# Kernel optimization log

Measured on AMD Instinct MI355X. Metric: run time of the kernel, lower is better.

## Reference

```python
import jax, jax.numpy as jnp
import numpy as np

B, NQ, NK, D, H = 2, 1024, 1024, 512, 32


def setup_inputs() -> dict:
    key = jax.random.key(0)
    ks = jax.random.split(key, 6)
    keys_t = jax.random.normal(ks[0], (B, NK, D), dtype=jnp.float32)
    queries = jax.random.normal(ks[1], (B, NQ, D), dtype=jnp.float32)
    # torch nn.Linear default init: U(-1/sqrt(fan_in), 1/sqrt(fan_in))
    s1 = 1.0 / np.sqrt(2 * D)
    W1 = jax.random.uniform(ks[2], (2 * D, H), jnp.float32, -s1, s1)  # (2d, hidden)
    b1 = jax.random.uniform(ks[3], (H,), jnp.float32, -s1, s1)
    s2 = 1.0 / np.sqrt(H)
    W2 = jax.random.uniform(ks[4], (H, 1), jnp.float32, -s2, s2)
    b2 = jax.random.uniform(ks[5], (1,), jnp.float32, -s2, s2)
    return {"keys": keys_t, "queries": queries, "W1": W1, "b1": b1, "W2": W2, "b2": b2}


def reference(keys, queries, W1, b1, W2, b2):
    # logits[b,q,k] = W2 . tanh(W1 @ cat(keys[b,k], queries[b,q]) + b1) + b2
    # Decompose first linear: cat(k,q) @ W1 == k @ W1[:D] + q @ W1[D:]
    d = keys.shape[-1]
    hk = jnp.einsum('bkd,dh->bkh', keys, W1[:d])      # (B, NK, H)
    hq = jnp.einsum('bqd,dh->bqh', queries, W1[d:])   # (B, NQ, H)
    h = jnp.tanh(hk[:, None, :, :] + hq[:, :, None, :] + b1)  # (B, NQ, NK, H)
    logits = jnp.einsum('bqkh,ho->bqko', h, W2)[..., 0] + b2[0]  # (B, NQ, NK)
    return logits
```

## Files before the change

### kernel.cpp

```cpp
#include <hip/hip_runtime.h>
#include <hip/hip_bf16.h>

#define NB 2
#define NQS 1024
#define NKS 1024
#define DD 512
#define HH 32
#define NKROW (NB * NKS)
#define W1S 34

typedef __attribute__((ext_vector_type(8))) short bf16x8;
typedef __attribute__((ext_vector_type(4))) float f32x4;

static __device__ __forceinline__ float fexp2(float x) {
#if __has_builtin(__builtin_amdgcn_exp2f)
  return __builtin_amdgcn_exp2f(x);
#else
  float r; asm("v_exp_f32 %0, %1" : "=v"(r) : "v"(x)); return r;
#endif
}
static __device__ __forceinline__ float frcp(float x) {
#if __has_builtin(__builtin_amdgcn_rcpf)
  return __builtin_amdgcn_rcpf(x);
#else
  float r; asm("v_rcp_f32 %0, %1" : "=v"(r) : "v"(x)); return r;
#endif
}
static __device__ __forceinline__ float rfl_f32(float x) {
  return __int_as_float(__builtin_amdgcn_readfirstlane(__float_as_int(x)));
}

__global__ __launch_bounds__(256) void p1_proj_mfma(
    const float* __restrict__ keys, const float* __restrict__ queries,
    const float* __restrict__ W1, const float* __restrict__ b1,
    float* __restrict__ E) {
  __shared__ __hip_bfloat16 W1L[DD * W1S];
  __shared__ float red[4 * 2 * 64 * 4];
  const float S = 2.8853900817779268f;
  const int tid = threadIdx.x;
  const int row0 = blockIdx.x * 16;
  const bool isq = row0 >= NKROW;
  const float* src = isq ? queries + (size_t)(row0 - NKROW) * DD
                         : keys + (size_t)row0 * DD;
  const float* w1 = W1 + (isq ? (size_t)DD * HH : 0);
#pragma unroll
  for (int s = 0; s < 16; ++s) {
    const int f = tid + s * 256;
    float4 v = *(const float4*)(w1 + (size_t)f * 4);
    const int k = f >> 3, h0 = (f & 7) * 4;
    __hip_bfloat16* p = &W1L[k * W1S + h0];
    p[0] = __float2bfloat16(v.x); p[1] = __float2bfloat16(v.y);
    p[2] = __float2bfloat16(v.z); p[3] = __float2bfloat16(v.w);
  }
  __syncthreads();
  const int l = tid & 63, w = tid >> 6;
  const int m = l & 15, kq = l >> 4;
  f32x4 acc0 = {0.f, 0.f, 0.f, 0.f}, acc1 = {0.f, 0.f, 0.f, 0.f};
  const float* arow = src + (size_t)m * DD + w * 128 + kq * 8;
  union Frag { bf16x8 v; __hip_bfloat16 e[8]; };
#pragma unroll
  for (int s = 0; s < 4; ++s) {
    const int kb = w * 128 + s * 32;
    float4 a0 = *(const float4*)(arow + s * 32);
    float4 a1 = *(const float4*)(arow + s * 32 + 4);
    Frag af, bf0, bf1;
    af.e[0] = __float2bfloat16(a0.x); af.e[1] = __float2bfloat16(a0.y);
    af.e[2] = __float2bfloat16(a0.z); af.e[3] = __float2bfloat16(a0.w);
    af.e[4] = __float2bfloat16(a1.x); af.e[5] = __float2bfloat16(a1.y);
    af.e[6] = __float2bfloat16(a1.z); af.e[7] = __float2bfloat16(a1.w);
    const __hip_bfloat16* bp = &W1L[(kb + kq * 8) * W1S + m];
#pragma unroll
    for (int j = 0; j < 8; ++j) {
      bf0.e[j] = bp[j * W1S];
      bf1.e[j] = bp[j * W1S + 16];
    }
    acc0 = __builtin_amdgcn_mfma_f32_16x16x32_bf16(af.v, bf0.v, acc0, 0, 0, 0);
    acc1 = __builtin_amdgcn_mfma_f32_16x16x32_bf16(af.v, bf1.v, acc1, 0, 0, 0);
  }
  *(f32x4*)(&red[((w * 2 + 0) * 64 + l) * 4]) = acc0;
  *(f32x4*)(&red[((w * 2 + 1) * 64 + l) * 4]) = acc1;
  __syncthreads();
#pragma unroll
  for (int u = 0; u < 2; ++u) {
    const int o = tid + u * 256;
    const int rr = o >> 5, h = o & 31;
    const int tt = h >> 4, mm = h & 15;
    const int ll = ((rr >> 2) << 4) | mm, r = rr & 3;
    float sum = red[(0 + tt) * 256 + ll * 4 + r] + red[(2 + tt) * 256 + ll * 4 + r] +
                red[(4 + tt) * 256 + ll * 4 + r] + red[(6 + tt) * 256 + ll * 4 + r];
    if (isq) sum += b1[h];
    E[(size_t)(row0 + rr) * HH + h] = fexp2(S * sum);
  }
}

__global__ __launch_bounds__(256, 4) void p2_score(
    const float* __restrict__ E, const float* __restrict__ W2,
    const float* __restrict__ b2, float* __restrict__ out) {
  const int tid = threadIdx.x;
  const int kl = tid & 63;
  const int qg = __builtin_amdgcn_readfirstlane(tid >> 6);
  const int k0 = blockIdx.x * 64, q0 = blockIdx.y * 32, b = blockIdx.z;
  float w2v[HH];
  float c0 = rfl_f32(b2[0]);
#pragma unroll
  for (int h = 0; h < HH; ++h) {
    w2v[h] = rfl_f32(W2[h]);
    c0 += w2v[h];
  }
  const float* ekp = E + (size_t)(b * NKS + k0 + kl) * HH;
  float acc[8];
#pragma unroll
  for (int j = 0; j < 8; ++j) acc[j] = c0;
#pragma unroll
  for (int half = 0; half < 2; ++half) {
    float ek[16];
#pragma unroll
    for (int i = 0; i < 4; ++i) {
      float4 v = *(const float4*)(ekp + half * 16 + i * 4);
      ek[i * 4 + 0] = v.x; ek[i * 4 + 1] = v.y;
      ek[i * 4 + 2] = v.z; ek[i * 4 + 3] = v.w;
    }
    const float* eqb =
        E + ((size_t)NKROW + (size_t)b * NQS + q0 + qg * 8) * HH + half * 16;
#pragma unroll
    for (int j = 0; j < 8; ++j) {
      const float* ej = eqb + (size_t)j * HH;
      float a0 = 0.f, a1 = 0.f;
#pragma unroll
      for (int i2 = 0; i2 < 4; ++i2) {
        float4 ev = *(const float4*)(ej + i2 * 4);
        const int hb = half * 16 + i2 * 4;
        {
          float da = fmaf(ek[i2 * 4 + 0], ev.x, 1.f);
          float db = fmaf(ek[i2 * 4 + 1], ev.y, 1.f);
          float num = fmaf(w2v[hb + 0], db, w2v[hb + 1] * da);
          a0 = fmaf(num, frcp(da * db), a0);
        }
        {
          float da = fmaf(ek[i2 * 4 + 2], ev.z, 1.f);
          float db = fmaf(ek[i2 * 4 + 3], ev.w, 1.f);
          float num = fmaf(w2v[hb + 2], db, w2v[hb + 3] * da);
          a1 = fmaf(num, frcp(da * db), a1);
        }
      }
      acc[j] = fmaf(-2.f, a0 + a1, acc[j]);
    }
  }
  float* outp = out + ((size_t)b * NQS + q0 + qg * 8) * NKS + k0 + kl;
#pragma unroll
  for (int j = 0; j < 8; ++j) outp[(size_t)j * NKS] = acc[j];
}

extern "C" void kernel_launch(void* const* d_in, const int* in_sizes, int n_in,
                              void* d_out, int out_size, void* d_ws, size_t ws_size,
                              hipStream_t stream) {
  const float* keys = (const float*)d_in[0];
  const float* queries = (const float*)d_in[1];
  const float* W1 = (const float*)d_in[2];
  const float* b1 = (const float*)d_in[3];
  const float* W2 = (const float*)d_in[4];
  const float* b2 = (const float*)d_in[5];
  float* out = (float*)d_out;
  float* ws = (float*)d_ws;

  hipLaunchKernelGGL(p1_proj_mfma, dim3(256), dim3(256), 0, stream,
                     keys, queries, W1, b1, ws);
  hipLaunchKernelGGL(p2_score, dim3(NKS / 64, NQS / 32, NB), dim3(256), 0, stream,
                     ws, W2, b2, out);
}
```

Before: 22.09 us.

## Fuse projection and scoring into one kernel with per-tile recomputed projections

Merges the projection kernel and the score kernel into a single launch. Each block projects its own 64 keys and 64 queries into shared memory with MFMA, then computes a 64x64 output tile, with a swizzled block order. This removes one launch and the global workspace round trip, but every block recomputes projections that other blocks share and re-stages W1 twice, which greatly increases redundant loads and MFMA work.

```diff
diff --git a/kernel.cpp b/kernel.cpp
--- a/kernel.cpp
+++ b/kernel.cpp
@@ -6,8 +6,8 @@
 #define NKS 1024
 #define DD 512
 #define HH 32
-#define NKROW (NB * NKS)
 #define W1S 34
+#define EKS 36
 
 typedef __attribute__((ext_vector_type(8))) short bf16x8;
 typedef __attribute__((ext_vector_type(4))) float f32x4;
@@ -30,76 +30,77 @@
   return __int_as_float(__builtin_amdgcn_readfirstlane(__float_as_int(x)));
 }
 
-__global__ __launch_bounds__(256) void p1_proj_mfma(
+__global__ __launch_bounds__(256) void fused_all(
     const float* __restrict__ keys, const float* __restrict__ queries,
     const float* __restrict__ W1, const float* __restrict__ b1,
-    float* __restrict__ E) {
+    const float* __restrict__ W2, const float* __restrict__ b2,
+    float* __restrict__ out) {
   __shared__ __hip_bfloat16 W1L[DD * W1S];
-  __shared__ float red[4 * 2 * 64 * 4];
+  __shared__ float EkL[64 * EKS];
+  __shared__ float EqL[64 * HH];
   const float S = 2.8853900817779268f;
   const int tid = threadIdx.x;
-  const int row0 = blockIdx.x * 16;
-  const bool isq = row0 >= NKROW;
-  const float* src = isq ? queries + (size_t)(row0 - NKROW) * DD
-                         : keys + (size_t)row0 * DD;
-  const float* w1 = W1 + (isq ? (size_t)DD * HH : 0);
-#pragma unroll
-  for (int s = 0; s < 16; ++s) {
-    const int f = tid + s * 256;
-    float4 v = *(const float4*)(w1 + (size_t)f * 4);
-    const int k = f >> 3, h0 = (f & 7) * 4;
-    __hip_bfloat16* p = &W1L[k * W1S + h0];
-    p[0] = __float2bfloat16(v.x); p[1] = __float2bfloat16(v.y);
-    p[2] = __float2bfloat16(v.z); p[3] = __float2bfloat16(v.w);
-  }
-  __syncthreads();
+  const int bid = blockIdx.x;
+  const int swz = (bid & 7) * 64 + (bid >> 3);
+  const int kt = swz >> 5, rem = swz & 31;
+  const int qt = rem >> 1, b = rem & 1;
   const int l = tid & 63, w = tid >> 6;
   const int m = l & 15, kq = l >> 4;
-  f32x4 acc0 = {0.f, 0.f, 0.f, 0.f}, acc1 = {0.f, 0.f, 0.f, 0.f};
-  const float* arow = src + (size_t)m * DD + w * 128 + kq * 8;
   union Frag { bf16x8 v; __hip_bfloat16 e[8]; };
+
 #pragma unroll
-  for (int s = 0; s < 4; ++s) {
-    const int kb = w * 128 + s * 32;
-    float4 a0 = *(const float4*)(arow + s * 32);
-    float4 a1 = *(const float4*)(arow + s * 32 + 4);
-    Frag af, bf0, bf1;
-    af.e[0] = __float2bfloat16(a0.x); af.e[1] = __float2bfloat16(a0.y);
-    af.e[2] = __float2bfloat16(a0.z); af.e[3] = __float2bfloat16(a0.w);
-    af.e[4] = __float2bfloat16(a1.x); af.e[5] = __float2bfloat16(a1.y);
-    af.e[6] = __float2bfloat16(a1.z); af.e[7] = __float2bfloat16(a1.w);
-    const __hip_bfloat16* bp = &W1L[(kb + kq * 8) * W1S + m];
+  for (int phase = 0; phase < 2; ++phase) {
+    const float* w1 = W1 + (size_t)phase * DD * HH;
 #pragma unroll
-    for (int j = 0; j < 8; ++j) {
-      bf0.e[j] = bp[j * W1S];
-      bf1.e[j] = bp[j * W1S + 16];
+    for (int s = 0; s < 16; ++s) {
+      const int f = tid + s * 256;
+      float4 v = *(const float4*)(w1 + (size_t)f * 4);
+      const int k = f >> 3, h0 = (f & 7) * 4;
+      __hip_bfloat16* p = &W1L[k * W1S + h0];
+      p[0] = __float2bfloat16(v.x); p[1] = __float2bfloat16(v.y);
+      p[2] = __float2bfloat16(v.z); p[3] = __float2bfloat16(v.w);
     }
-    acc0 = __builtin_amdgcn_mfma_f32_16x16x32_bf16(af.v, bf0.v, acc0, 0, 0, 0);
-    acc1 = __builtin_amdgcn_mfma_f32_16x16x32_bf16(af.v, bf1.v, acc1, 0, 0, 0);
+    __syncthreads();
+    const float* src = phase ? queries + (size_t)(b * NQS + qt * 64 + w * 16 + m) * DD
+                             : keys + (size_t)(b * NKS + kt * 64 + w * 16 + m) * DD;
+    const float* arow = src + kq * 8;
+    f32x4 acc0 = {0.f, 0.f, 0.f, 0.f}, acc1 = {0.f, 0.f, 0.f, 0.f};
+#pragma unroll
+    for (int s = 0; s < 16; ++s) {
+      float4 a0 = *(const float4*)(arow + s * 32);
+      float4 a1 = *(const float4*)(arow + s * 32 + 4);
+      Frag af, bf0, bf1;
+      af.e[0] = __float2bfloat16(a0.x); af.e[1] = __float2bfloat16(a0.y);
+      af.e[2] = __float2bfloat16(a0.z); af.e[3] = __float2bfloat16(a0.w);
+      af.e[4] = __float2bfloat16(a1.x); af.e[5] = __float2bfloat16(a1.y);
+      af.e[6] = __float2bfloat16(a1.z); af.e[7] = __float2bfloat16(a1.w);
+      const __hip_bfloat16* bp = &W1L[(s * 32 + kq * 8) * W1S + m];
+#pragma unroll
+      for (int j = 0; j < 8; ++j) {
+        bf0.e[j] = bp[j * W1S];
+        bf1.e[j] = bp[j * W1S + 16];
+      }
+      acc0 = __builtin_amdgcn_mfma_f32_16x16x32_bf16(af.v, bf0.v, acc0, 0, 0, 0);
+      acc1 = __builtin_amdgcn_mfma_f32_16x16x32_bf16(af.v, bf1.v, acc1, 0, 0, 0);
+    }
+    if (phase == 0) {
+#pragma unroll
+      for (int r = 0; r < 4; ++r) {
+        const int rr = w * 16 + kq * 4 + r;
+        EkL[rr * EKS + m] = fexp2(S * acc0[r]);
+        EkL[rr * EKS + 16 + m] = fexp2(S * acc1[r]);
+      }
+    } else {
+      const float bias0 = b1[m], bias1 = b1[16 + m];
+#pragma unroll
+      for (int r = 0; r < 4; ++r) {
+        const int rr = w * 16 + kq * 4 + r;
+        EqL[rr * HH + m] = fexp2(S * (acc0[r] + bias0));
+        EqL[rr * HH + 16 + m] = fexp2(S * (acc1[r] + bias1));
+      }
+    }
+    __syncthreads();
   }
-  *(f32x4*)(&red[((w * 2 + 0) * 64 + l) * 4]) = acc0;
-  *(f32x4*)(&red[((w * 2 + 1) * 64 + l) * 4]) = acc1;
-  __syncthreads();
-#pragma unroll
-  for (int u = 0; u < 2; ++u) {
-    const int o = tid + u * 256;
-    const int rr = o >> 5, h = o & 31;
-    const int tt = h >> 4, mm = h & 15;
-    const int ll = ((rr >> 2) << 4) | mm, r = rr & 3;
-    float sum = red[(0 + tt) * 256 + ll * 4 + r] + red[(2 + tt) * 256 + ll * 4 + r] +
-                red[(4 + tt) * 256 + ll * 4 + r] + red[(6 + tt) * 256 + ll * 4 + r];
-    if (isq) sum += b1[h];
-    E[(size_t)(row0 + rr) * HH + h] = fexp2(S * sum);
-  }
-}
-
-__global__ __launch_bounds__(256, 4) void p2_score(
-    const float* __restrict__ E, const float* __restrict__ W2,
-    const float* __restrict__ b2, float* __restrict__ out) {
-  const int tid = threadIdx.x;
-  const int kl = tid & 63;
-  const int qg = __builtin_amdgcn_readfirstlane(tid >> 6);
-  const int k0 = blockIdx.x * 64, q0 = blockIdx.y * 32, b = blockIdx.z;
   float w2v[HH];
   float c0 = rfl_f32(b2[0]);
 #pragma unroll
@@ -107,48 +108,39 @@
     w2v[h] = rfl_f32(W2[h]);
     c0 += w2v[h];
   }
-  const float* ekp = E + (size_t)(b * NKS + k0 + kl) * HH;
-  float acc[8];
+  const int kl = l;
+  float ek[HH];
 #pragma unroll
-  for (int j = 0; j < 8; ++j) acc[j] = c0;
+  for (int i = 0; i < 8; ++i) {
+    float4 v = *(const float4*)(&EkL[kl * EKS + i * 4]);
+    ek[i * 4 + 0] = v.x; ek[i * 4 + 1] = v.y;
+    ek[i * 4 + 2] = v.z; ek[i * 4 + 3] = v.w;
+  }
+  float* outp = out + ((size_t)b * NQS + qt * 64 + w * 16) * NKS + kt * 64 + kl;
+#pragma unroll 4
+  for (int j = 0; j < 16; ++j) {
+    const float* ej = &EqL[(w * 16 + j) * HH];
+    float a0 = 0.f, a1 = 0.f;
 #pragma unroll
-  for (int half = 0; half < 2; ++half) {
-    float ek[16];
-#pragma unroll
-    for (int i = 0; i < 4; ++i) {
-      float4 v = *(const float4*)(ekp + half * 16 + i * 4);
-      ek[i * 4 + 0] = v.x; ek[i * 4 + 1] = v.y;
-      ek[i * 4 + 2] = v.z; ek[i * 4 + 3] = v.w;
+    for (int i2 = 0; i2 < 8; ++i2) {
+      float4 ev = *(const float4*)(ej + i2 * 4);
+      {
+        const int hb = i2 * 4;
+        float da = fmaf(ek[hb + 0], ev.x, 1.f);
+        float db = fmaf(ek[hb + 1], ev.y, 1.f);
+        float num = fmaf(w2v[hb + 0], db, w2v[hb + 1] * da);
+        a0 = fmaf(num, frcp(da * db), a0);
+      }
+      {
+        const int hb = i2 * 4 + 2;
+        float da = fmaf(ek[hb + 0], ev.z, 1.f);
+        float db = fmaf(ek[hb + 1], ev.w, 1.f);
+        float num = fmaf(w2v[hb + 0], db, w2v[hb + 1] * da);
+        a1 = fmaf(num, frcp(da * db), a1);
+      }
     }
-    const float* eqb =
-        E + ((size_t)NKROW + (size_t)b * NQS + q0 + qg * 8) * HH + half * 16;
-#pragma unroll
-    for (int j = 0; j < 8; ++j) {
-      const float* ej = eqb + (size_t)j * HH;
-      float a0 = 0.f, a1 = 0.f;
-#pragma unroll
-      for (int i2 = 0; i2 < 4; ++i2) {
-        float4 ev = *(const float4*)(ej + i2 * 4);
-        const int hb = half * 16 + i2 * 4;
-        {
-          float da = fmaf(ek[i2 * 4 + 0], ev.x, 1.f);
-          float db = fmaf(ek[i2 * 4 + 1], ev.y, 1.f);
-          float num = fmaf(w2v[hb + 0], db, w2v[hb + 1] * da);
-          a0 = fmaf(num, frcp(da * db), a0);
-        }
-        {
-          float da = fmaf(ek[i2 * 4 + 2], ev.z, 1.f);
-          float db = fmaf(ek[i2 * 4 + 3], ev.w, 1.f);
-          float num = fmaf(w2v[hb + 2], db, w2v[hb + 3] * da);
-          a1 = fmaf(num, frcp(da * db), a1);
-        }
-      }
-      acc[j] = fmaf(-2.f, a0 + a1, acc[j]);
-    }
+    outp[(size_t)j * NKS] = fmaf(-2.f, a0 + a1, c0);
   }
-  float* outp = out + ((size_t)b * NQS + q0 + qg * 8) * NKS + k0 + kl;
-#pragma unroll
-  for (int j = 0; j < 8; ++j) outp[(size_t)j * NKS] = acc[j];
 }
 
 extern "C" void kernel_launch(void* const* d_in, const int* in_sizes, int n_in,
@@ -161,10 +153,7 @@
   const float* W2 = (const float*)d_in[4];
   const float* b2 = (const float*)d_in[5];
   float* out = (float*)d_out;
-  float* ws = (float*)d_ws;
 
-  hipLaunchKernelGGL(p1_proj_mfma, dim3(256), dim3(256), 0, stream,
-                     keys, queries, W1, b1, ws);
-  hipLaunchKernelGGL(p2_score, dim3(NKS / 64, NQS / 32, NB), dim3(256), 0, stream,
-                     ws, W2, b2, out);
+  hipLaunchKernelGGL(fused_all, dim3(512), dim3(256), 0, stream,
+                     keys, queries, W1, b1, W2, b2, out);
 }
```

New measurement: 30.79 us. 39.4% more time.

## Split projection K-dimension across blocks and halve per-block query tile in scoring

Applied to the files above, without the earlier changes.

The projection kernel is split into a partial stage where each block handles one 128-wide chunk of the reduction dimension (1024 blocks instead of 256), plus a separate finish kernel that sums the four partials, adds bias and applies exp2. The scoring kernel now processes 16 queries per block instead of 32, doubling the grid, and applies the constant and -2 scale at store time. The aim is more parallelism and better CU fill on the small projection, and higher occupancy in scoring. In exchange it adds a kernel launch and an extra global round trip for the partial sums, and each scoring block reloads key data for less work.

```diff
diff --git a/kernel.cpp b/kernel.cpp
--- a/kernel.cpp
+++ b/kernel.cpp
@@ -30,21 +30,20 @@
   return __int_as_float(__builtin_amdgcn_readfirstlane(__float_as_int(x)));
 }
 
-__global__ __launch_bounds__(256) void p1_proj_mfma(
+__global__ __launch_bounds__(256) void p1a_partial(
     const float* __restrict__ keys, const float* __restrict__ queries,
-    const float* __restrict__ W1, const float* __restrict__ b1,
-    float* __restrict__ E) {
-  __shared__ __hip_bfloat16 W1L[DD * W1S];
+    const float* __restrict__ W1, float* __restrict__ Epart) {
+  __shared__ __hip_bfloat16 W1L[128 * W1S];
   __shared__ float red[4 * 2 * 64 * 4];
-  const float S = 2.8853900817779268f;
   const int tid = threadIdx.x;
-  const int row0 = blockIdx.x * 16;
+  const int rt = blockIdx.x >> 2, kc = blockIdx.x & 3;
+  const int row0 = rt * 16;
   const bool isq = row0 >= NKROW;
   const float* src = isq ? queries + (size_t)(row0 - NKROW) * DD
                          : keys + (size_t)row0 * DD;
-  const float* w1 = W1 + (isq ? (size_t)DD * HH : 0);
+  const float* w1 = W1 + (isq ? (size_t)DD * HH : 0) + (size_t)kc * 128 * HH;
 #pragma unroll
-  for (int s = 0; s < 16; ++s) {
+  for (int s = 0; s < 4; ++s) {
     const int f = tid + s * 256;
     float4 v = *(const float4*)(w1 + (size_t)f * 4);
     const int k = f >> 3, h0 = (f & 7) * 4;
@@ -55,28 +54,24 @@
   __syncthreads();
   const int l = tid & 63, w = tid >> 6;
   const int m = l & 15, kq = l >> 4;
-  f32x4 acc0 = {0.f, 0.f, 0.f, 0.f}, acc1 = {0.f, 0.f, 0.f, 0.f};
-  const float* arow = src + (size_t)m * DD + w * 128 + kq * 8;
   union Frag { bf16x8 v; __hip_bfloat16 e[8]; };
+  const float* arow = src + (size_t)m * DD + kc * 128 + w * 32 + kq * 8;
+  float4 a0 = *(const float4*)(arow);
+  float4 a1 = *(const float4*)(arow + 4);
+  Frag af, bf0, bf1;
+  af.e[0] = __float2bfloat16(a0.x); af.e[1] = __float2bfloat16(a0.y);
+  af.e[2] = __float2bfloat16(a0.z); af.e[3] = __float2bfloat16(a0.w);
+  af.e[4] = __float2bfloat16(a1.x); af.e[5] = __float2bfloat16(a1.y);
+  af.e[6] = __float2bfloat16(a1.z); af.e[7] = __float2bfloat16(a1.w);
+  const __hip_bfloat16* bp = &W1L[(w * 32 + kq * 8) * W1S + m];
 #pragma unroll
-  for (int s = 0; s < 4; ++s) {
-    const int kb = w * 128 + s * 32;
-    float4 a0 = *(const float4*)(arow + s * 32);
-    float4 a1 = *(const float4*)(arow + s * 32 + 4);
-    Frag af, bf0, bf1;
-    af.e[0] = __float2bfloat16(a0.x); af.e[1] = __float2bfloat16(a0.y);
-    af.e[2] = __float2bfloat16(a0.z); af.e[3] = __float2bfloat16(a0.w);
-    af.e[4] = __float2bfloat16(a1.x); af.e[5] = __float2bfloat16(a1.y);
-    af.e[6] = __float2bfloat16(a1.z); af.e[7] = __float2bfloat16(a1.w);
-    const __hip_bfloat16* bp = &W1L[(kb + kq * 8) * W1S + m];
-#pragma unroll
-    for (int j = 0; j < 8; ++j) {
-      bf0.e[j] = bp[j * W1S];
-      bf1.e[j] = bp[j * W1S + 16];
-    }
-    acc0 = __builtin_amdgcn_mfma_f32_16x16x32_bf16(af.v, bf0.v, acc0, 0, 0, 0);
-    acc1 = __builtin_amdgcn_mfma_f32_16x16x32_bf16(af.v, bf1.v, acc1, 0, 0, 0);
+  for (int j = 0; j < 8; ++j) {
+    bf0.e[j] = bp[j * W1S];
+    bf1.e[j] = bp[j * W1S + 16];
   }
+  f32x4 z = {0.f, 0.f, 0.f, 0.f};
+  f32x4 acc0 = __builtin_amdgcn_mfma_f32_16x16x32_bf16(af.v, bf0.v, z, 0, 0, 0);
+  f32x4 acc1 = __builtin_amdgcn_mfma_f32_16x16x32_bf16(af.v, bf1.v, z, 0, 0, 0);
   *(f32x4*)(&red[((w * 2 + 0) * 64 + l) * 4]) = acc0;
   *(f32x4*)(&red[((w * 2 + 1) * 64 + l) * 4]) = acc1;
   __syncthreads();
@@ -88,9 +83,20 @@
     const int ll = ((rr >> 2) << 4) | mm, r = rr & 3;
     float sum = red[(0 + tt) * 256 + ll * 4 + r] + red[(2 + tt) * 256 + ll * 4 + r] +
                 red[(4 + tt) * 256 + ll * 4 + r] + red[(6 + tt) * 256 + ll * 4 + r];
-    if (isq) sum += b1[h];
-    E[(size_t)(row0 + rr) * HH + h] = fexp2(S * sum);
+    Epart[((size_t)kc * 4096 + row0 + rr) * HH + h] = sum;
   }
+}
+
+__global__ __launch_bounds__(256) void p1b_finish(
+    const float* __restrict__ Epart, const float* __restrict__ b1,
+    float* __restrict__ E) {
+  const float S = 2.8853900817779268f;
+  const int o = blockIdx.x * 256 + threadIdx.x;
+  const int row = o >> 5, h = o & 31;
+  float sum = Epart[(size_t)o] + Epart[(size_t)o + 4096 * HH] +
+              Epart[(size_t)o + 2 * 4096 * HH] + Epart[(size_t)o + 3 * 4096 * HH];
+  if (row >= NKROW) sum += b1[h];
+  E[(size_t)o] = fexp2(S * sum);
 }
 
 __global__ __launch_bounds__(256, 4) void p2_score(
@@ -99,7 +105,7 @@
   const int tid = threadIdx.x;
   const int kl = tid & 63;
   const int qg = __builtin_amdgcn_readfirstlane(tid >> 6);
-  const int k0 = blockIdx.x * 64, q0 = blockIdx.y * 32, b = blockIdx.z;
+  const int k0 = blockIdx.x * 64, q0 = blockIdx.y * 16, b = blockIdx.z;
   float w2v[HH];
   float c0 = rfl_f32(b2[0]);
 #pragma unroll
@@ -108,9 +114,7 @@
     c0 += w2v[h];
   }
   const float* ekp = E + (size_t)(b * NKS + k0 + kl) * HH;
-  float acc[8];
-#pragma unroll
-  for (int j = 0; j < 8; ++j) acc[j] = c0;
+  float acc[4] = {0.f, 0.f, 0.f, 0.f};
 #pragma unroll
   for (int half = 0; half < 2; ++half) {
     float ek[16];
@@ -121,9 +125,9 @@
       ek[i * 4 + 2] = v.z; ek[i * 4 + 3] = v.w;
     }
     const float* eqb =
-        E + ((size_t)NKROW + (size_t)b * NQS + q0 + qg * 8) * HH + half * 16;
+        E + ((size_t)NKROW + (size_t)b * NQS + q0 + qg * 4) * HH + half * 16;
 #pragma unroll
-    for (int j = 0; j < 8; ++j) {
+    for (int j = 0; j < 4; ++j) {
       const float* ej = eqb + (size_t)j * HH;
       float a0 = 0.f, a1 = 0.f;
 #pragma unroll
@@ -143,12 +147,12 @@
           a1 = fmaf(num, frcp(da * db), a1);
         }
       }
-      acc[j] = fmaf(-2.f, a0 + a1, acc[j]);
+      acc[j] += a0 + a1;
     }
   }
-  float* outp = out + ((size_t)b * NQS + q0 + qg * 8) * NKS + k0 + kl;
+  float* outp = out + ((size_t)b * NQS + q0 + qg * 4) * NKS + k0 + kl;
 #pragma unroll
-  for (int j = 0; j < 8; ++j) outp[(size_t)j * NKS] = acc[j];
+  for (int j = 0; j < 4; ++j) outp[(size_t)j * NKS] = fmaf(-2.f, acc[j], c0);
 }
 
 extern "C" void kernel_launch(void* const* d_in, const int* in_sizes, int n_in,
@@ -162,9 +166,13 @@
   const float* b2 = (const float*)d_in[5];
   float* out = (float*)d_out;
   float* ws = (float*)d_ws;
+  float* E = ws;
+  float* Epart = ws + 1024 * 1024;
 
-  hipLaunchKernelGGL(p1_proj_mfma, dim3(256), dim3(256), 0, stream,
-                     keys, queries, W1, b1, ws);
-  hipLaunchKernelGGL(p2_score, dim3(NKS / 64, NQS / 32, NB), dim3(256), 0, stream,
-                     ws, W2, b2, out);
+  hipLaunchKernelGGL(p1a_partial, dim3(1024), dim3(256), 0, stream,
+                     keys, queries, W1, Epart);
+  hipLaunchKernelGGL(p1b_finish, dim3(512), dim3(256), 0, stream,
+                     Epart, b1, E);
+  hipLaunchKernelGGL(p2_score, dim3(NKS / 64, NQS / 16, NB), dim3(256), 0, stream,
+                     E, W2, b2, out);
 }
```

Measured after the change: 24.34 us. +10.2%, slower.
